# Kernel optimization log

Hardware: AMD Instinct MI355X
Metric: run time of the kernel (lower is better)

## Reference

```python
import jax, jax.numpy as jnp
import numpy as np

B, L, D = 128, 512, 512   # batch, len_max, encoder feature dim
E, H, V = 64, 512, 17     # label emb size, hidden size, label vocab
PAD = 0                   # entl_pad_value


def setup_inputs() -> dict:
    key = jax.random.key(0)
    ks = jax.random.split(key, 6)
    inputs = jax.random.normal(ks[0], (B, L, D), dtype=jnp.float32)
    emb_table = jax.random.normal(ks[1], (V, E), dtype=jnp.float32) * 0.02
    # xavier_uniform with tanh gain for ht1
    gain = 5.0 / 3.0
    limit1 = gain * np.sqrt(6.0 / (D + E + H))
    W1 = jax.random.uniform(ks[2], (H, D + E), dtype=jnp.float32,
                            minval=-limit1, maxval=limit1)
    b1 = jnp.zeros((H,), dtype=jnp.float32)
    limit2 = np.sqrt(1.0 / H)
    W2 = jax.random.uniform(ks[3], (V, H), dtype=jnp.float32,
                            minval=-limit2, maxval=limit2)
    b2 = jax.random.uniform(ks[4], (V,), dtype=jnp.float32,
                            minval=-limit2, maxval=limit2)
    return {"inputs": inputs, "emb_table": emb_table,
            "W1": W1, "b1": b1, "W2": W2, "b2": b2}


def reference(inputs, emb_table, W1, b1, W2, b2):
    # padding_idx row is identically zero (as in nn.Embedding(padding_idx=PAD))
    table = emb_table.at[PAD].set(0.0)

    def step(prev_emb, x_t):
        # x_t: [B, D], prev_emb: [B, E]
        x = jnp.concatenate([x_t, prev_emb], axis=-1)          # [B, D+E]
        h = jnp.tanh(x @ W1.T + b1)                            # [B, H]
        logit = h @ W2.T + b2                                  # [B, V]
        logp = jax.nn.log_softmax(logit, axis=-1)              # [B, V]
        pred = jnp.argmax(logp, axis=-1)                       # [B] int
        emb = table[pred]                                      # [B, E]
        return emb, (logit, pred, logp, emb)

    init_emb = jnp.broadcast_to(table[PAD], (inputs.shape[0], E))
    xs = jnp.swapaxes(inputs, 0, 1)                            # [L, B, D]
    _, (logits, preds, probs, preds_emb) = jax.lax.scan(step, init_emb, xs)
    # stack along time -> move time to dim 1
    logits = jnp.swapaxes(logits, 0, 1)       # [B, L, V]
    preds = jnp.swapaxes(preds, 0, 1)         # [B, L]
    probs = jnp.swapaxes(probs, 0, 1)         # [B, L, V]
    preds_emb = jnp.swapaxes(preds_emb, 0, 1) # [B, L, E]
    return logits, preds, probs, preds_emb
```

## Files before the change

kernel.cpp:

```cpp
#include <hip/hip_runtime.h>
#include <math.h>

#define B_ 128
#define L_ 512
#define D_ 512
#define E_ 64
#define H_ 512
#define V_ 17

#define LOG2E_F 1.4426950408889634f
#define LN2_F   0.6931471805599453f

__device__ __forceinline__ float fast_tanh(float x) {
  float e = __builtin_amdgcn_exp2f(x * (2.0f * LOG2E_F));
  return 1.0f - 2.0f * __builtin_amdgcn_rcpf(e + 1.0f);
}

__global__ void dh_kernel(const float* __restrict__ W1, const float* __restrict__ table,
                          float* __restrict__ TD) {
  int h = threadIdx.x;
  float w[E_];
#pragma unroll
  for (int e = 0; e < E_; ++e) w[e] = W1[h * (D_ + E_) + D_ + e];
  TD[h] = 0.f;
  for (int v = 1; v < V_; ++v) {
    float acc = 0.f;
#pragma unroll
    for (int e = 0; e < E_; ++e) acc += w[e] * table[v * E_ + e];
    TD[v * H_ + h] = fast_tanh(acc);
  }
}

#define PITCH 20
#define SCALE_A 1024.0f
#define SCALE_W 256.0f
#define INV_SCALE (1.0f / (1024.0f * 256.0f))

typedef _Float16 half8 __attribute__((ext_vector_type(8)));
typedef __fp16 fp16x2 __attribute__((ext_vector_type(2)));
typedef float float4v __attribute__((ext_vector_type(4)));

union H8c { half8 h; fp16x2 q[4]; unsigned int u[4]; uint4 u4; };

__device__ __forceinline__ uint4 split4(float4 v, float scale) {
  float a0 = v.x * scale, a1 = v.y * scale, a2 = v.z * scale, a3 = v.w * scale;
  _Float16 h0 = (_Float16)a0, h1 = (_Float16)a1, h2 = (_Float16)a2, h3 = (_Float16)a3;
  _Float16 l0 = (_Float16)(a0 - (float)h0), l1 = (_Float16)(a1 - (float)h1);
  _Float16 l2 = (_Float16)(a2 - (float)h2), l3 = (_Float16)(a3 - (float)h3);
  union { _Float16 h; unsigned short u; } c;
  unsigned int hu0, hu1, hu2, hu3, lu0, lu1, lu2, lu3;
  c.h = h0; hu0 = c.u; c.h = h1; hu1 = c.u; c.h = h2; hu2 = c.u; c.h = h3; hu3 = c.u;
  c.h = l0; lu0 = c.u; c.h = l1; lu1 = c.u; c.h = l2; lu2 = c.u; c.h = l3; lu3 = c.u;
  uint4 r;
  r.x = hu0 | (hu1 << 16);
  r.y = hu2 | (hu3 << 16);
  r.z = lu0 | (lu1 << 16);
  r.w = lu2 | (lu3 << 16);
  return r;
}

__device__ __forceinline__ uint2 pack4h(_Float16 a, _Float16 b, _Float16 c, _Float16 d) {
  union { _Float16 h; unsigned short u; } x;
  unsigned int lo, hi;
  x.h = a; lo = x.u; x.h = b; lo |= ((unsigned int)x.u) << 16;
  x.h = c; hi = x.u; x.h = d; hi |= ((unsigned int)x.u) << 16;
  return make_uint2(lo, hi);
}

__global__ __launch_bounds__(256)
void wsplit_kernel(const float* __restrict__ W1, unsigned int* __restrict__ WHI,
                   unsigned int* __restrict__ WLO) {
  const int idx = blockIdx.x * 256 + threadIdx.x;
  const int row = idx >> 7, c4 = idx & 127;
  const float4 wv = *(const float4*)&W1[(size_t)row * (D_ + E_) + 4 * c4];
  const uint4 pw = split4(wv, SCALE_W);
  *(uint2*)&WHI[row * 256 + 2 * c4] = make_uint2(pw.x, pw.y);
  *(uint2*)&WLO[row * 256 + 2 * c4] = make_uint2(pw.z, pw.w);
}

__global__ __launch_bounds__(512, 2)
void gemm_kernel(const float* __restrict__ A, const unsigned int* __restrict__ WHI,
                 const unsigned int* __restrict__ WLO,
                 const float* __restrict__ b1, float* __restrict__ TZ) {
  __shared__ unsigned int Ahi[128 * PITCH], Alo[128 * PITCH];
  __shared__ unsigned int Whi[512 * PITCH], Wlo[512 * PITCH];

  const int t = threadIdx.x;
  const int ln = t & 63, w = t >> 6;
  const int wm = w & 1, wn = w >> 1;
  const int mBase = blockIdx.x * 128;
  const int lrow = ln & 15, lquad = ln >> 4;

  float4v acc[4][8];
#pragma unroll
  for (int i = 0; i < 4; ++i)
#pragma unroll
    for (int j = 0; j < 8; ++j) acc[i][j] = (float4v){0.f, 0.f, 0.f, 0.f};

  for (int kt = 0; kt < D_; kt += 32) {
#pragma unroll
    for (int q = 0; q < 2; ++q) {
      const int idx = q * 512 + t;
      const int m = idx >> 3, f = idx & 7;
      const float4 av = *(const float4*)&A[(size_t)(mBase + m) * D_ + kt + 4 * f];
      const uint4 pa = split4(av, SCALE_A);
      *(uint2*)&Ahi[m * PITCH + 2 * f] = make_uint2(pa.x, pa.y);
      *(uint2*)&Alo[m * PITCH + 2 * f] = make_uint2(pa.z, pa.w);
    }
#pragma unroll
    for (int q = 0; q < 4; ++q) {
      const int idx = q * 512 + t;
      const int n = idx >> 2, d4 = (idx & 3) * 4;
      *(uint4*)&Whi[n * PITCH + d4] = *(const uint4*)&WHI[n * 256 + (kt >> 1) + d4];
      *(uint4*)&Wlo[n * PITCH + d4] = *(const uint4*)&WLO[n * 256 + (kt >> 1) + d4];
    }
    __syncthreads();

    half8 ah[4], al[4];
#pragma unroll
    for (int tm = 0; tm < 4; ++tm) {
      const int off = (wm * 64 + tm * 16 + lrow) * PITCH + 4 * lquad;
      ah[tm] = *(const half8*)&Ahi[off];
      al[tm] = *(const half8*)&Alo[off];
    }
#pragma unroll
    for (int tn = 0; tn < 8; ++tn) {
      const int off = (wn * 128 + tn * 16 + lrow) * PITCH + 4 * lquad;
      const half8 bh = *(const half8*)&Whi[off];
      const half8 bl = *(const half8*)&Wlo[off];
#pragma unroll
      for (int tm = 0; tm < 4; ++tm) {
        acc[tm][tn] = __builtin_amdgcn_mfma_f32_16x16x32_f16(ah[tm], bh, acc[tm][tn], 0, 0, 0);
        acc[tm][tn] = __builtin_amdgcn_mfma_f32_16x16x32_f16(ah[tm], bl, acc[tm][tn], 0, 0, 0);
        acc[tm][tn] = __builtin_amdgcn_mfma_f32_16x16x32_f16(al[tm], bh, acc[tm][tn], 0, 0, 0);
      }
    }
    __syncthreads();
  }

#pragma unroll
  for (int tn = 0; tn < 8; ++tn) {
    const int col = wn * 128 + tn * 16 + lrow;
    const float bv = b1[col];
#pragma unroll
    for (int tm = 0; tm < 4; ++tm) {
      const int row0 = mBase + wm * 64 + tm * 16 + lquad * 4;
#pragma unroll
      for (int r = 0; r < 4; ++r)
        TZ[(size_t)(row0 + r) * H_ + col] = fast_tanh(acc[tm][tn][r] * INV_SCALE + bv);
    }
  }
}

#define LGR 32
#define AP 520
#define WP 260

__global__ __launch_bounds__(512, 2)
void lg_kernel(const float* Zin, const float* __restrict__ TD,
               const float* __restrict__ W2, const float* __restrict__ b2,
               float* G) {
  __shared__ __align__(16) unsigned int sAhiD[LGR * AP / 2];
  __shared__ __align__(16) unsigned int sAloD[LGR * AP / 2];
  __shared__ __align__(16) unsigned int sUD[LGR * AP / 2];
  __shared__ __align__(16) unsigned int sTDd[V_ * 256];
  __shared__ __align__(16) unsigned int sW2hi[16 * WP];
  __shared__ __align__(16) unsigned int sW2lo[16 * WP];
  __shared__ __align__(16) unsigned int sW16hi[256];
  __shared__ __align__(16) unsigned int sW16lo[256];
  __shared__ __align__(16) float sS[8][16][20];
  __shared__ __align__(16) float sV16b[32];
  __shared__ __align__(16) unsigned char nb[LGR][20];

  const int t = threadIdx.x;
  const int ln = t & 63, w = t >> 6;
  const int bt0 = blockIdx.x * LGR;

#pragma unroll
  for (int i = 0; i < 8; ++i) {
    const int f = t + 512 * i;
    const int r = f >> 7, c4 = f & 127;
    const float4 z = *(const float4*)&Zin[(size_t)(bt0 + r) * H_ + 4 * c4];
    const float a0 = 1024.f * z.x, a1 = 1024.f * z.y, a2 = 1024.f * z.z, a3 = 1024.f * z.w;
    const _Float16 h0 = (_Float16)a0, h1 = (_Float16)a1, h2 = (_Float16)a2, h3 = (_Float16)a3;
    const _Float16 l0 = (_Float16)(a0 - (float)h0), l1 = (_Float16)(a1 - (float)h1);
    const _Float16 l2 = (_Float16)(a2 - (float)h2), l3 = (_Float16)(a3 - (float)h3);
    const _Float16 u0 = (_Float16)fmaf(-a0, z.x, 1024.f), u1 = (_Float16)fmaf(-a1, z.y, 1024.f);
    const _Float16 u2 = (_Float16)fmaf(-a2, z.z, 1024.f), u3 = (_Float16)fmaf(-a3, z.w, 1024.f);
    const int o = r * (AP / 2) + 2 * c4;
    *(uint2*)&sAhiD[o] = pack4h(h0, h1, h2, h3);
    *(uint2*)&sAloD[o] = pack4h(l0, l1, l2, l3);
    *(uint2*)&sUD[o]   = pack4h(u0, u1, u2, u3);
  }
#pragma unroll
  for (int i = 0; i < 5; ++i) {
    const int f = t + 512 * i;
    if (f < V_ * 128) {
      const int r = f >> 7, c4 = f & 127;
      const float4 d = *(const float4*)&TD[(size_t)r * H_ + 4 * c4];
      *(uint2*)&sTDd[r * 256 + 2 * c4] =
          pack4h((_Float16)d.x, (_Float16)d.y, (_Float16)d.z, (_Float16)d.w);
    }
  }
#pragma unroll
  for (int i = 0; i < 4; ++i) {
    const int f = t + 512 * i;
    const int r = f >> 7, c4 = f & 127;
    const float4 wv = *(const float4*)&W2[(size_t)r * H_ + 4 * c4];
    const uint4 pw = split4(wv, SCALE_W);
    *(uint2*)&sW2hi[r * WP + 2 * c4] = make_uint2(pw.x, pw.y);
    *(uint2*)&sW2lo[r * WP + 2 * c4] = make_uint2(pw.z, pw.w);
  }
  if (t < 128) {
    const float4 wv = *(const float4*)&W2[(size_t)16 * H_ + 4 * t];
    const uint4 pw = split4(wv, 1.0f);
    *(uint2*)&sW16hi[2 * t] = make_uint2(pw.x, pw.y);
    *(uint2*)&sW16lo[2 * t] = make_uint2(pw.z, pw.w);
  }
  __syncthreads();

  {
    const int row = t >> 4, seg = t & 15;
    const unsigned int* Ah = &sAhiD[row * (AP / 2) + seg * 16];
    const unsigned int* Al = &sAloD[row * (AP / 2) + seg * 16];
    const unsigned int* Wh = &sW16hi[seg * 16];
    const unsigned int* Wl = &sW16lo[seg * 16];
    float s = 0.f;
#pragma unroll
    for (int j = 0; j < 16; ++j) {
      const fp16x2 a = __builtin_bit_cast(fp16x2, Ah[j]);
      const fp16x2 l = __builtin_bit_cast(fp16x2, Al[j]);
      const fp16x2 wh = __builtin_bit_cast(fp16x2, Wh[j]);
      const fp16x2 wl = __builtin_bit_cast(fp16x2, Wl[j]);
      s = __builtin_amdgcn_fdot2(a, wh, s, false);
      s = __builtin_amdgcn_fdot2(l, wh, s, false);
      s = __builtin_amdgcn_fdot2(a, wl, s, false);
    }
    ((float*)sS)[row * 16 + seg] = s;
  }
  __syncthreads();
  if (t < 32) {
    float s = 0.f;
#pragma unroll
    for (int j = 0; j < 16; ++j) s += ((float*)sS)[t * 16 + j];
    sV16b[t] = s;
  }
  __syncthreads();

  const int lrow = ln & 15, lq = ln >> 4;
  const int rg = w & 1, pq = w >> 1;
  const int rbase = rg * 16;
  const float b2a = b2[lrow];
  const float b2c = b2[16];

  float4v acc[5];
  float p16s[5];
#pragma unroll
  for (int pi = 0; pi < 5; ++pi) { acc[pi] = (float4v){0.f, 0.f, 0.f, 0.f}; p16s[pi] = 0.f; }

  const _Float16* Ahalf = (const _Float16*)sAhiD;
  const _Float16* Alhalf = (const _Float16*)sAloD;
  const _Float16* Uhalf = (const _Float16*)sUD;
  const _Float16* TDhalf = (const _Float16*)sTDd;

  for (int kt = 0; kt < H_; kt += 32) {
    const int ho = kt + lq * 8;
    const half8 ahi = *(const half8*)(Ahalf + (rbase + lrow) * AP + ho);
    const half8 alo = *(const half8*)(Alhalf + (rbase + lrow) * AP + ho);
    const half8 uu  = *(const half8*)(Uhalf + (rbase + lrow) * AP + ho);
    const half8 tzv = ahi * (_Float16)0.0009765625f;
    H8c W16f; W16f.u4 = *(const uint4*)&sW16hi[ho >> 1];
    const int wo = lrow * WP + (kt >> 1) + lq * 4;
    const half8 bh0 = *(const half8*)&sW2hi[wo];
    const half8 bl0 = *(const half8*)&sW2lo[wo];
#pragma unroll
    for (int pi = 0; pi < 5; ++pi) {
      const int p = pq + 4 * pi;
      if (p < V_) {
        const half8 td = *(const half8*)(TDhalf + p * 512 + ho);
        const half8 q = tzv * td;
        const half8 s = q * q + ((_Float16)1.0f - q);
        const half8 dl = uu * (td * s);
        const half8 alp = alo + dl;
        acc[pi] = __builtin_amdgcn_mfma_f32_16x16x32_f16(ahi, bh0, acc[pi], 0, 0, 0);
        acc[pi] = __builtin_amdgcn_mfma_f32_16x16x32_f16(ahi, bl0, acc[pi], 0, 0, 0);
        acc[pi] = __builtin_amdgcn_mfma_f32_16x16x32_f16(alp, bh0, acc[pi], 0, 0, 0);
        H8c DL; DL.h = dl;
        p16s[pi] = __builtin_amdgcn_fdot2(DL.q[0], W16f.q[0], p16s[pi], false);
        p16s[pi] = __builtin_amdgcn_fdot2(DL.q[1], W16f.q[1], p16s[pi], false);
        p16s[pi] = __builtin_amdgcn_fdot2(DL.q[2], W16f.q[2], p16s[pi], false);
        p16s[pi] = __builtin_amdgcn_fdot2(DL.q[3], W16f.q[3], p16s[pi], false);
      }
    }
  }

#pragma unroll
  for (int pi = 0; pi < 5; ++pi) {
    const int p = pq + 4 * pi;
    if (p < V_) {
      float p16 = p16s[pi];
      p16 += __shfl_xor(p16, 16, 64);
      p16 += __shfl_xor(p16, 32, 64);
#pragma unroll
      for (int r = 0; r < 4; ++r)
        sS[w][lq * 4 + r][lrow] = acc[pi][r] * INV_SCALE + b2a;
      if (ln < 16) {
        float va[17];
        const float4 q0 = *(const float4*)&sS[w][ln][0];
        const float4 q1 = *(const float4*)&sS[w][ln][4];
        const float4 q2 = *(const float4*)&sS[w][ln][8];
        const float4 q3 = *(const float4*)&sS[w][ln][12];
        va[0] = q0.x; va[1] = q0.y; va[2] = q0.z; va[3] = q0.w;
        va[4] = q1.x; va[5] = q1.y; va[6] = q1.z; va[7] = q1.w;
        va[8] = q2.x; va[9] = q2.y; va[10] = q2.z; va[11] = q2.w;
        va[12] = q3.x; va[13] = q3.y; va[14] = q3.z; va[15] = q3.w;
        va[16] = (sV16b[rbase + ln] + p16) * 0.0009765625f + b2c;
        float m = va[0]; int am = 0;
#pragma unroll
        for (int i = 1; i < 17; ++i) if (va[i] > m) { m = va[i]; am = i; }
        float* gs = &G[(size_t)(bt0 + rbase + ln) * H_ + p * 20];
        *(float4*)&gs[0] = q0; *(float4*)&gs[4] = q1;
        *(float4*)&gs[8] = q2; *(float4*)&gs[12] = q3;
        gs[16] = va[16];
        nb[rbase + ln][p] = (unsigned char)am;
      }
    }
  }
  __syncthreads();
  if (t < 160) {
    const int row = t / 5, d = t % 5;
    ((unsigned int*)&G[(size_t)(bt0 + row) * H_ + 352])[d] =
        *(const unsigned int*)&nb[row][d * 4];
  }
}

__global__ __launch_bounds__(64, 1)
void chase_kernel(const float* __restrict__ G, float* __restrict__ out_preds) {
  __shared__ unsigned char nxt[L_ * 32];
  const int b = blockIdx.x, ln = threadIdx.x;
#pragma unroll
  for (int i = 0; i < 8; ++i) {
    const int tt = ln + 64 * i;
    const unsigned int* src = (const unsigned int*)&G[((size_t)b * L_ + tt) * H_ + 352];
    *(uint4*)&nxt[tt * 32] = *(const uint4*)src;
    *(unsigned int*)&nxt[tt * 32 + 16] = src[4];
  }
  __syncthreads();
  int pred = 0;
  float* op = out_preds + (size_t)b * L_;
  for (int tt = 0; tt < L_; ++tt) {
    pred = nxt[tt * 32 + pred];
    if (ln == 0) op[tt] = (float)pred;
  }
}

__global__ __launch_bounds__(256)
void epi_kernel(const float* __restrict__ G, const float* __restrict__ table,
                const float* __restrict__ preds,
                float* __restrict__ out_logits, float* __restrict__ out_probs,
                float* __restrict__ out_pemb) {
  const int bt = blockIdx.x * 256 + threadIdx.x;
  const int tt = bt & (L_ - 1);
  const int p = (tt == 0) ? 0 : (int)preds[bt - 1];
  const float* g = &G[(size_t)bt * H_ + p * 20];
  float va[17];
  {
    const float4 q0 = *(const float4*)&g[0];
    const float4 q1 = *(const float4*)&g[4];
    const float4 q2 = *(const float4*)&g[8];
    const float4 q3 = *(const float4*)&g[12];
    va[0] = q0.x; va[1] = q0.y; va[2] = q0.z; va[3] = q0.w;
    va[4] = q1.x; va[5] = q1.y; va[6] = q1.z; va[7] = q1.w;
    va[8] = q2.x; va[9] = q2.y; va[10] = q2.z; va[11] = q2.w;
    va[12] = q3.x; va[13] = q3.y; va[14] = q3.z; va[15] = q3.w;
    va[16] = g[16];
  }
  float m = va[0];
#pragma unroll
  for (int i = 1; i < 17; ++i) m = fmaxf(m, va[i]);
  float s = 0.f;
#pragma unroll
  for (int i = 0; i < 17; ++i) s += __builtin_amdgcn_exp2f((va[i] - m) * LOG2E_F);
  const float lse = __builtin_amdgcn_logf(s) * LN2_F;
  float* lo = out_logits + (size_t)bt * V_;
  float* pb = out_probs + (size_t)bt * V_;
#pragma unroll
  for (int i = 0; i < 17; ++i) { lo[i] = va[i]; pb[i] = va[i] - m - lse; }
  const int pr = (int)preds[bt];
  float* pe = out_pemb + (size_t)bt * E_;
  if (pr == 0) {
#pragma unroll
    for (int i = 0; i < 16; ++i) *(float4*)&pe[4 * i] = (float4){0.f, 0.f, 0.f, 0.f};
  } else {
    const float* tr = &table[(size_t)pr * E_];
#pragma unroll
    for (int i = 0; i < 16; ++i) *(float4*)&pe[4 * i] = *(const float4*)&tr[4 * i];
  }
}

extern "C" void kernel_launch(void* const* d_in, const int* in_sizes, int n_in,
                              void* d_out, int out_size, void* d_ws, size_t ws_size,
                              hipStream_t stream) {
  const float* inputs = (const float*)d_in[0];
  const float* table  = (const float*)d_in[1];
  const float* W1     = (const float*)d_in[2];
  const float* b1     = (const float*)d_in[3];
  const float* W2     = (const float*)d_in[4];
  const float* b2     = (const float*)d_in[5];

  float* out = (float*)d_out;
  float* out_logits = out;
  float* out_preds  = out_logits + (size_t)B_ * L_ * V_;
  float* out_probs  = out_preds + (size_t)B_ * L_;
  float* out_pemb   = out_probs + (size_t)B_ * L_ * V_;

  float* TD = (float*)d_ws;
  float* TZ = (float*)((char*)d_ws + 65536);

  unsigned int* WHI = (unsigned int*)out_pemb;
  unsigned int* WLO = WHI + 512 * 256;

  dh_kernel<<<1, 512, 0, stream>>>(W1, table, TD);
  wsplit_kernel<<<256, 256, 0, stream>>>(W1, WHI, WLO);
  gemm_kernel<<<512, 512, 0, stream>>>(inputs, WHI, WLO, b1, TZ);
  lg_kernel<<<65536 / LGR, 512, 0, stream>>>(TZ, TD, W2, b2, TZ);
  chase_kernel<<<B_, 64, 0, stream>>>(TZ, out_preds);
  epi_kernel<<<65536 / 256, 256, 0, stream>>>(TZ, table, out_preds,
                                              out_logits, out_probs, out_pemb);
}
```

Baseline: 502.4 us.

## Recast per-predecessor logit correction as a precomputed-weight MFMA GEMM

```diff
diff --git a/kernel.cpp b/kernel.cpp
--- a/kernel.cpp
+++ b/kernel.cpp
@@ -16,31 +16,14 @@
   return 1.0f - 2.0f * __builtin_amdgcn_rcpf(e + 1.0f);
 }
 
-__global__ void dh_kernel(const float* __restrict__ W1, const float* __restrict__ table,
-                          float* __restrict__ TD) {
-  int h = threadIdx.x;
-  float w[E_];
-#pragma unroll
-  for (int e = 0; e < E_; ++e) w[e] = W1[h * (D_ + E_) + D_ + e];
-  TD[h] = 0.f;
-  for (int v = 1; v < V_; ++v) {
-    float acc = 0.f;
-#pragma unroll
-    for (int e = 0; e < E_; ++e) acc += w[e] * table[v * E_ + e];
-    TD[v * H_ + h] = fast_tanh(acc);
-  }
-}
-
 #define PITCH 20
 #define SCALE_A 1024.0f
 #define SCALE_W 256.0f
 #define INV_SCALE (1.0f / (1024.0f * 256.0f))
+#define NC 304
 
 typedef _Float16 half8 __attribute__((ext_vector_type(8)));
-typedef __fp16 fp16x2 __attribute__((ext_vector_type(2)));
 typedef float float4v __attribute__((ext_vector_type(4)));
-
-union H8c { half8 h; fp16x2 q[4]; unsigned int u[4]; uint4 u4; };
 
 __device__ __forceinline__ uint4 split4(float4 v, float scale) {
   float a0 = v.x * scale, a1 = v.y * scale, a2 = v.z * scale, a3 = v.w * scale;
@@ -59,23 +42,61 @@
   return r;
 }
 
-__device__ __forceinline__ uint2 pack4h(_Float16 a, _Float16 b, _Float16 c, _Float16 d) {
-  union { _Float16 h; unsigned short u; } x;
-  unsigned int lo, hi;
-  x.h = a; lo = x.u; x.h = b; lo |= ((unsigned int)x.u) << 16;
-  x.h = c; hi = x.u; x.h = d; hi |= ((unsigned int)x.u) << 16;
-  return make_uint2(lo, hi);
+__device__ __forceinline__ unsigned int pack2h(float a, float b) {
+  union { _Float16 h; unsigned short u; } x, y;
+  x.h = (_Float16)a; y.h = (_Float16)b;
+  return (unsigned int)x.u | ((unsigned int)y.u << 16);
 }
 
 __global__ __launch_bounds__(256)
-void wsplit_kernel(const float* __restrict__ W1, unsigned int* __restrict__ WHI,
-                   unsigned int* __restrict__ WLO) {
-  const int idx = blockIdx.x * 256 + threadIdx.x;
-  const int row = idx >> 7, c4 = idx & 127;
-  const float4 wv = *(const float4*)&W1[(size_t)row * (D_ + E_) + 4 * c4];
-  const uint4 pw = split4(wv, SCALE_W);
-  *(uint2*)&WHI[row * 256 + 2 * c4] = make_uint2(pw.x, pw.y);
-  *(uint2*)&WLO[row * 256 + 2 * c4] = make_uint2(pw.z, pw.w);
+void prep_kernel(const float* __restrict__ W1, const float* __restrict__ W2,
+                 const float* __restrict__ table,
+                 unsigned int* __restrict__ WHI, unsigned int* __restrict__ WLO,
+                 unsigned int* __restrict__ W2HI, unsigned int* __restrict__ W2LO,
+                 unsigned int* __restrict__ Kp, unsigned int* __restrict__ K2p) {
+  const int bid = blockIdx.x, t = threadIdx.x;
+  if (bid < 256) {
+    const int idx = bid * 256 + t;
+    const int row = idx >> 7, c4 = idx & 127;
+    const float4 wv = *(const float4*)&W1[(size_t)row * (D_ + E_) + 4 * c4];
+    const uint4 pw = split4(wv, SCALE_W);
+    *(uint2*)&WHI[row * 256 + 2 * c4] = make_uint2(pw.x, pw.y);
+    *(uint2*)&WLO[row * 256 + 2 * c4] = make_uint2(pw.z, pw.w);
+  } else if (bid < 265) {
+    const int i = (bid - 256) * 256 + t;
+    if (i < V_ * 128) {
+      const int row = i >> 7, c4 = i & 127;
+      const float4 wv = *(const float4*)&W2[(size_t)row * H_ + 4 * c4];
+      const uint4 pw = split4(wv, SCALE_W);
+      *(uint2*)&W2HI[row * 256 + 2 * c4] = make_uint2(pw.x, pw.y);
+      *(uint2*)&W2LO[row * 256 + 2 * c4] = make_uint2(pw.z, pw.w);
+    }
+  } else {
+    const int c = bid - 265;
+    unsigned int o1 = 0, o2 = 0;
+    if (c < 289) {
+      const int p = c / 17, v = c - p * 17;
+      float k1[2], k2[2];
+#pragma unroll
+      for (int s = 0; s < 2; ++s) {
+        const int h = 2 * t + s;
+        float td = 0.f;
+        if (p > 0) {
+          float acc = 0.f;
+          for (int e = 0; e < E_; ++e)
+            acc += W1[(size_t)h * (D_ + E_) + D_ + e] * table[p * E_ + e];
+          td = fast_tanh(acc);
+        }
+        const float w2v = W2[(size_t)v * H_ + h];
+        k1[s] = 256.0f * td * w2v;
+        k2[s] = 65536.0f * td * td * w2v;
+      }
+      o1 = pack2h(k1[0], k1[1]);
+      o2 = pack2h(k2[0], k2[1]);
+    }
+    Kp[c * 256 + t] = o1;
+    K2p[c * 256 + t] = o2;
+  }
 }
 
 __global__ __launch_bounds__(512, 2)
@@ -152,185 +173,182 @@
   }
 }
 
-#define LGR 32
-#define AP 520
-#define WP 260
-
-__global__ __launch_bounds__(512, 2)
-void lg_kernel(const float* Zin, const float* __restrict__ TD,
-               const float* __restrict__ W2, const float* __restrict__ b2,
-               float* G) {
-  __shared__ __align__(16) unsigned int sAhiD[LGR * AP / 2];
-  __shared__ __align__(16) unsigned int sAloD[LGR * AP / 2];
-  __shared__ __align__(16) unsigned int sUD[LGR * AP / 2];
-  __shared__ __align__(16) unsigned int sTDd[V_ * 256];
-  __shared__ __align__(16) unsigned int sW2hi[16 * WP];
-  __shared__ __align__(16) unsigned int sW2lo[16 * WP];
-  __shared__ __align__(16) unsigned int sW16hi[256];
-  __shared__ __align__(16) unsigned int sW16lo[256];
-  __shared__ __align__(16) float sS[8][16][20];
-  __shared__ __align__(16) float sV16b[32];
-  __shared__ __align__(16) unsigned char nb[LGR][20];
+__global__ __launch_bounds__(512, 1)
+void glog_kernel(const float* Zin, const unsigned int* __restrict__ KpD,
+                 const unsigned int* __restrict__ K2D,
+                 const unsigned int* __restrict__ W2HI, const unsigned int* __restrict__ W2LO,
+                 const float* __restrict__ b2, float* G) {
+  __shared__ __align__(16) char pool[97408];
+  unsigned int* Ahi = (unsigned int*)pool;
+  unsigned int* Alo = Ahi + 2560;
+  unsigned int* Uf  = Alo + 2560;
+  unsigned int* A2f = Uf + 2560;
+  unsigned int* Bc  = A2f + 2560;
+  unsigned int* Bc2 = Bc + 6080;
+  unsigned int* Bh  = Bc2 + 6080;
+  unsigned int* Bl  = Bh + 640;
 
   const int t = threadIdx.x;
   const int ln = t & 63, w = t >> 6;
-  const int bt0 = blockIdx.x * LGR;
-
-#pragma unroll
-  for (int i = 0; i < 8; ++i) {
-    const int f = t + 512 * i;
-    const int r = f >> 7, c4 = f & 127;
-    const float4 z = *(const float4*)&Zin[(size_t)(bt0 + r) * H_ + 4 * c4];
-    const float a0 = 1024.f * z.x, a1 = 1024.f * z.y, a2 = 1024.f * z.z, a3 = 1024.f * z.w;
-    const _Float16 h0 = (_Float16)a0, h1 = (_Float16)a1, h2 = (_Float16)a2, h3 = (_Float16)a3;
-    const _Float16 l0 = (_Float16)(a0 - (float)h0), l1 = (_Float16)(a1 - (float)h1);
-    const _Float16 l2 = (_Float16)(a2 - (float)h2), l3 = (_Float16)(a3 - (float)h3);
-    const _Float16 u0 = (_Float16)fmaf(-a0, z.x, 1024.f), u1 = (_Float16)fmaf(-a1, z.y, 1024.f);
-    const _Float16 u2 = (_Float16)fmaf(-a2, z.z, 1024.f), u3 = (_Float16)fmaf(-a3, z.w, 1024.f);
-    const int o = r * (AP / 2) + 2 * c4;
-    *(uint2*)&sAhiD[o] = pack4h(h0, h1, h2, h3);
-    *(uint2*)&sAloD[o] = pack4h(l0, l1, l2, l3);
-    *(uint2*)&sUD[o]   = pack4h(u0, u1, u2, u3);
-  }
-#pragma unroll
-  for (int i = 0; i < 5; ++i) {
-    const int f = t + 512 * i;
-    if (f < V_ * 128) {
-      const int r = f >> 7, c4 = f & 127;
-      const float4 d = *(const float4*)&TD[(size_t)r * H_ + 4 * c4];
-      *(uint2*)&sTDd[r * 256 + 2 * c4] =
-          pack4h((_Float16)d.x, (_Float16)d.y, (_Float16)d.z, (_Float16)d.w);
-    }
-  }
-#pragma unroll
-  for (int i = 0; i < 4; ++i) {
-    const int f = t + 512 * i;
-    const int r = f >> 7, c4 = f & 127;
-    const float4 wv = *(const float4*)&W2[(size_t)r * H_ + 4 * c4];
-    const uint4 pw = split4(wv, SCALE_W);
-    *(uint2*)&sW2hi[r * WP + 2 * c4] = make_uint2(pw.x, pw.y);
-    *(uint2*)&sW2lo[r * WP + 2 * c4] = make_uint2(pw.z, pw.w);
-  }
-  if (t < 128) {
-    const float4 wv = *(const float4*)&W2[(size_t)16 * H_ + 4 * t];
-    const uint4 pw = split4(wv, 1.0f);
-    *(uint2*)&sW16hi[2 * t] = make_uint2(pw.x, pw.y);
-    *(uint2*)&sW16lo[2 * t] = make_uint2(pw.z, pw.w);
-  }
-  __syncthreads();
-
-  {
-    const int row = t >> 4, seg = t & 15;
-    const unsigned int* Ah = &sAhiD[row * (AP / 2) + seg * 16];
-    const unsigned int* Al = &sAloD[row * (AP / 2) + seg * 16];
-    const unsigned int* Wh = &sW16hi[seg * 16];
-    const unsigned int* Wl = &sW16lo[seg * 16];
-    float s = 0.f;
-#pragma unroll
-    for (int j = 0; j < 16; ++j) {
-      const fp16x2 a = __builtin_bit_cast(fp16x2, Ah[j]);
-      const fp16x2 l = __builtin_bit_cast(fp16x2, Al[j]);
-      const fp16x2 wh = __builtin_bit_cast(fp16x2, Wh[j]);
-      const fp16x2 wl = __builtin_bit_cast(fp16x2, Wl[j]);
-      s = __builtin_amdgcn_fdot2(a, wh, s, false);
-      s = __builtin_amdgcn_fdot2(l, wh, s, false);
-      s = __builtin_amdgcn_fdot2(a, wl, s, false);
-    }
-    ((float*)sS)[row * 16 + seg] = s;
-  }
-  __syncthreads();
-  if (t < 32) {
-    float s = 0.f;
-#pragma unroll
-    for (int j = 0; j < 16; ++j) s += ((float*)sS)[t * 16 + j];
-    sV16b[t] = s;
-  }
-  __syncthreads();
-
+  const int wm = w & 1, wn = w >> 1;
   const int lrow = ln & 15, lq = ln >> 4;
-  const int rg = w & 1, pq = w >> 1;
-  const int rbase = rg * 16;
-  const float b2a = b2[lrow];
-  const float b2c = b2[16];
-
-  float4v acc[5];
-  float p16s[5];
-#pragma unroll
-  for (int pi = 0; pi < 5; ++pi) { acc[pi] = (float4v){0.f, 0.f, 0.f, 0.f}; p16s[pi] = 0.f; }
-
-  const _Float16* Ahalf = (const _Float16*)sAhiD;
-  const _Float16* Alhalf = (const _Float16*)sAloD;
-  const _Float16* Uhalf = (const _Float16*)sUD;
-  const _Float16* TDhalf = (const _Float16*)sTDd;
+  const int bt0 = blockIdx.x * 128;
+
+  if (t < 300) { Bh[340 + t] = 0; Bl[340 + t] = 0; }
+
+  float4v accC[5][4];
+  float4v accB[2][4];
+#pragma unroll
+  for (int i = 0; i < 5; ++i)
+#pragma unroll
+    for (int mt = 0; mt < 4; ++mt) accC[i][mt] = (float4v){0.f, 0.f, 0.f, 0.f};
+#pragma unroll
+  for (int i = 0; i < 2; ++i)
+#pragma unroll
+    for (int mt = 0; mt < 4; ++mt) accB[i][mt] = (float4v){0.f, 0.f, 0.f, 0.f};
 
   for (int kt = 0; kt < H_; kt += 32) {
-    const int ho = kt + lq * 8;
-    const half8 ahi = *(const half8*)(Ahalf + (rbase + lrow) * AP + ho);
-    const half8 alo = *(const half8*)(Alhalf + (rbase + lrow) * AP + ho);
-    const half8 uu  = *(const half8*)(Uhalf + (rbase + lrow) * AP + ho);
-    const half8 tzv = ahi * (_Float16)0.0009765625f;
-    H8c W16f; W16f.u4 = *(const uint4*)&sW16hi[ho >> 1];
-    const int wo = lrow * WP + (kt >> 1) + lq * 4;
-    const half8 bh0 = *(const half8*)&sW2hi[wo];
-    const half8 bl0 = *(const half8*)&sW2lo[wo];
-#pragma unroll
-    for (int pi = 0; pi < 5; ++pi) {
-      const int p = pq + 4 * pi;
-      if (p < V_) {
-        const half8 td = *(const half8*)(TDhalf + p * 512 + ho);
-        const half8 q = tzv * td;
-        const half8 s = q * q + ((_Float16)1.0f - q);
-        const half8 dl = uu * (td * s);
-        const half8 alp = alo + dl;
-        acc[pi] = __builtin_amdgcn_mfma_f32_16x16x32_f16(ahi, bh0, acc[pi], 0, 0, 0);
-        acc[pi] = __builtin_amdgcn_mfma_f32_16x16x32_f16(ahi, bl0, acc[pi], 0, 0, 0);
-        acc[pi] = __builtin_amdgcn_mfma_f32_16x16x32_f16(alp, bh0, acc[pi], 0, 0, 0);
-        H8c DL; DL.h = dl;
-        p16s[pi] = __builtin_amdgcn_fdot2(DL.q[0], W16f.q[0], p16s[pi], false);
-        p16s[pi] = __builtin_amdgcn_fdot2(DL.q[1], W16f.q[1], p16s[pi], false);
-        p16s[pi] = __builtin_amdgcn_fdot2(DL.q[2], W16f.q[2], p16s[pi], false);
-        p16s[pi] = __builtin_amdgcn_fdot2(DL.q[3], W16f.q[3], p16s[pi], false);
-      }
-    }
-  }
-
-#pragma unroll
-  for (int pi = 0; pi < 5; ++pi) {
-    const int p = pq + 4 * pi;
-    if (p < V_) {
-      float p16 = p16s[pi];
-      p16 += __shfl_xor(p16, 16, 64);
-      p16 += __shfl_xor(p16, 32, 64);
-#pragma unroll
-      for (int r = 0; r < 4; ++r)
-        sS[w][lq * 4 + r][lrow] = acc[pi][r] * INV_SCALE + b2a;
-      if (ln < 16) {
-        float va[17];
-        const float4 q0 = *(const float4*)&sS[w][ln][0];
-        const float4 q1 = *(const float4*)&sS[w][ln][4];
-        const float4 q2 = *(const float4*)&sS[w][ln][8];
-        const float4 q3 = *(const float4*)&sS[w][ln][12];
-        va[0] = q0.x; va[1] = q0.y; va[2] = q0.z; va[3] = q0.w;
-        va[4] = q1.x; va[5] = q1.y; va[6] = q1.z; va[7] = q1.w;
-        va[8] = q2.x; va[9] = q2.y; va[10] = q2.z; va[11] = q2.w;
-        va[12] = q3.x; va[13] = q3.y; va[14] = q3.z; va[15] = q3.w;
-        va[16] = (sV16b[rbase + ln] + p16) * 0.0009765625f + b2c;
-        float m = va[0]; int am = 0;
-#pragma unroll
-        for (int i = 1; i < 17; ++i) if (va[i] > m) { m = va[i]; am = i; }
-        float* gs = &G[(size_t)(bt0 + rbase + ln) * H_ + p * 20];
-        *(float4*)&gs[0] = q0; *(float4*)&gs[4] = q1;
-        *(float4*)&gs[8] = q2; *(float4*)&gs[12] = q3;
-        gs[16] = va[16];
-        nb[rbase + ln][p] = (unsigned char)am;
-      }
-    }
-  }
-  __syncthreads();
-  if (t < 160) {
-    const int row = t / 5, d = t % 5;
-    ((unsigned int*)&G[(size_t)(bt0 + row) * H_ + 352])[d] =
-        *(const unsigned int*)&nb[row][d * 4];
+#pragma unroll
+    for (int i = 0; i < 2; ++i) {
+      const int idx = i * 512 + t;
+      const int m = idx >> 3, f = idx & 7;
+      const float4 z = *(const float4*)&Zin[(size_t)(bt0 + m) * H_ + kt + 4 * f];
+      const uint4 pa = split4(z, SCALE_A);
+      *(uint2*)&Ahi[m * PITCH + 2 * f] = make_uint2(pa.x, pa.y);
+      *(uint2*)&Alo[m * PITCH + 2 * f] = make_uint2(pa.z, pa.w);
+      const float u0 = fmaf(-z.x, z.x, 1.0f), u1 = fmaf(-z.y, z.y, 1.0f);
+      const float u2 = fmaf(-z.z, z.z, 1.0f), u3 = fmaf(-z.w, z.w, 1.0f);
+      *(uint2*)&Uf[m * PITCH + 2 * f] = make_uint2(pack2h(u0, u1), pack2h(u2, u3));
+      const float s2 = -1.0f / 256.0f;
+      *(uint2*)&A2f[m * PITCH + 2 * f] =
+          make_uint2(pack2h(u0 * z.x * s2, u1 * z.y * s2),
+                     pack2h(u2 * z.z * s2, u3 * z.w * s2));
+    }
+#pragma unroll
+    for (int i = 0; i < 3; ++i) {
+      const int idx = i * 512 + t;
+      if (idx < NC * 4) {
+        const int c = idx >> 2, g4 = (idx & 3) * 4;
+        *(uint4*)&Bc[c * PITCH + g4]  = *(const uint4*)&KpD[c * 256 + (kt >> 1) + g4];
+        *(uint4*)&Bc2[c * PITCH + g4] = *(const uint4*)&K2D[c * 256 + (kt >> 1) + g4];
+      }
+    }
+    if (t < 68) {
+      const int v = t >> 2, g4 = (t & 3) * 4;
+      *(uint4*)&Bh[v * PITCH + g4] = *(const uint4*)&W2HI[v * 256 + (kt >> 1) + g4];
+    } else if (t < 136) {
+      const int t2 = t - 68, v = t2 >> 2, g4 = (t2 & 3) * 4;
+      *(uint4*)&Bl[v * PITCH + g4] = *(const uint4*)&W2LO[v * 256 + (kt >> 1) + g4];
+    }
+    __syncthreads();
+
+    half8 fa_hi[4], fa_lo[4], fa_u[4], fa_a2[4];
+#pragma unroll
+    for (int mt = 0; mt < 4; ++mt) {
+      const int off = (wm * 64 + mt * 16 + lrow) * PITCH + 4 * lq;
+      fa_hi[mt] = *(const half8*)&Ahi[off];
+      fa_lo[mt] = *(const half8*)&Alo[off];
+      fa_u[mt]  = *(const half8*)&Uf[off];
+      fa_a2[mt] = *(const half8*)&A2f[off];
+    }
+#pragma unroll
+    for (int i = 0; i < 5; ++i) {
+      if (wn < 3 || i < 4) {
+        const int c = (wn * 5 + i) * 16 + lrow;
+        const half8 fb  = *(const half8*)&Bc[c * PITCH + 4 * lq];
+        const half8 fb2 = *(const half8*)&Bc2[c * PITCH + 4 * lq];
+#pragma unroll
+        for (int mt = 0; mt < 4; ++mt) {
+          accC[i][mt] = __builtin_amdgcn_mfma_f32_16x16x32_f16(fa_u[mt], fb, accC[i][mt], 0, 0, 0);
+          accC[i][mt] = __builtin_amdgcn_mfma_f32_16x16x32_f16(fa_a2[mt], fb2, accC[i][mt], 0, 0, 0);
+        }
+      }
+    }
+    if (wn == 3) {
+#pragma unroll
+      for (int bt2 = 0; bt2 < 2; ++bt2) {
+        const int off = (bt2 * 16 + lrow) * PITCH + 4 * lq;
+        const half8 bh = *(const half8*)&Bh[off];
+        const half8 bl = *(const half8*)&Bl[off];
+#pragma unroll
+        for (int mt = 0; mt < 4; ++mt) {
+          accB[bt2][mt] = __builtin_amdgcn_mfma_f32_16x16x32_f16(fa_hi[mt], bh, accB[bt2][mt], 0, 0, 0);
+          accB[bt2][mt] = __builtin_amdgcn_mfma_f32_16x16x32_f16(fa_hi[mt], bl, accB[bt2][mt], 0, 0, 0);
+          accB[bt2][mt] = __builtin_amdgcn_mfma_f32_16x16x32_f16(fa_lo[mt], bh, accB[bt2][mt], 0, 0, 0);
+        }
+      }
+    }
+    __syncthreads();
+  }
+
+  float* Gbuf = (float*)pool;
+  float* Bb   = Gbuf + 64 * 353;
+  float* sb2  = Bb + 64 * 21;
+  unsigned char* nbb = (unsigned char*)(sb2 + 20);
+
+  if (t < V_) sb2[t] = b2[t];
+
+#pragma unroll
+  for (int half = 0; half < 2; ++half) {
+    if (half) __syncthreads();
+    if (wm == half) {
+#pragma unroll
+      for (int i = 0; i < 5; ++i) {
+        if (wn < 3 || i < 4) {
+          const int c = (wn * 5 + i) * 16 + lrow;
+          if (c < 289) {
+            const int p = c / 17, v = c - p * 17;
+            const int j = p * 20 + v;
+#pragma unroll
+            for (int mt = 0; mt < 4; ++mt)
+#pragma unroll
+              for (int r = 0; r < 4; ++r)
+                Gbuf[(mt * 16 + lq * 4 + r) * 353 + j] = accC[i][mt][r] * (1.0f / 256.0f);
+          }
+        }
+      }
+      if (wn == 3) {
+#pragma unroll
+        for (int bt2 = 0; bt2 < 2; ++bt2) {
+          const int v = bt2 * 16 + lrow;
+          if (v < V_) {
+#pragma unroll
+            for (int mt = 0; mt < 4; ++mt)
+#pragma unroll
+              for (int r = 0; r < 4; ++r)
+                Bb[(mt * 16 + lq * 4 + r) * 21 + v] = accB[bt2][mt][r] * INV_SCALE;
+          }
+        }
+      }
+    }
+    __syncthreads();
+#pragma unroll
+    for (int k = 0; k < 3; ++k) {
+      const int task = k * 512 + t;
+      if (task < 1088) {
+        const int row = task & 63, p = task >> 6;
+        float g[17];
+#pragma unroll
+        for (int v = 0; v < V_; ++v)
+          g[v] = Gbuf[row * 353 + p * 20 + v] + Bb[row * 21 + v] + sb2[v];
+        float m = g[0]; int am = 0;
+#pragma unroll
+        for (int v = 1; v < V_; ++v) if (g[v] > m) { m = g[v]; am = v; }
+        float* gs = &G[(size_t)(bt0 + half * 64 + row) * H_ + p * 20];
+        *(float4*)&gs[0]  = make_float4(g[0], g[1], g[2], g[3]);
+        *(float4*)&gs[4]  = make_float4(g[4], g[5], g[6], g[7]);
+        *(float4*)&gs[8]  = make_float4(g[8], g[9], g[10], g[11]);
+        *(float4*)&gs[12] = make_float4(g[12], g[13], g[14], g[15]);
+        gs[16] = g[16];
+        nbb[row * 20 + p] = (unsigned char)am;
+      }
+    }
+    __syncthreads();
+    if (t < 320) {
+      const int row = t / 5, d = t % 5;
+      ((unsigned int*)&G[(size_t)(bt0 + half * 64 + row) * H_ + 352])[d] =
+          *(const unsigned int*)&nbb[row * 20 + 4 * d];
+    }
   }
 }
 
@@ -377,15 +395,15 @@
   }
   float m = va[0];
 #pragma unroll
-  for (int i = 1; i < 17; ++i) m = fmaxf(m, va[i]);
+  for (int i = 1; i < V_; ++i) m = fmaxf(m, va[i]);
   float s = 0.f;
 #pragma unroll
-  for (int i = 0; i < 17; ++i) s += __builtin_amdgcn_exp2f((va[i] - m) * LOG2E_F);
+  for (int i = 0; i < V_; ++i) s += __builtin_amdgcn_exp2f((va[i] - m) * LOG2E_F);
   const float lse = __builtin_amdgcn_logf(s) * LN2_F;
   float* lo = out_logits + (size_t)bt * V_;
   float* pb = out_probs + (size_t)bt * V_;
 #pragma unroll
-  for (int i = 0; i < 17; ++i) { lo[i] = va[i]; pb[i] = va[i] - m - lse; }
+  for (int i = 0; i < V_; ++i) { lo[i] = va[i]; pb[i] = va[i] - m - lse; }
   const int pr = (int)preds[bt];
   float* pe = out_pemb + (size_t)bt * E_;
   if (pr == 0) {
@@ -414,16 +432,18 @@
   float* out_probs  = out_preds + (size_t)B_ * L_;
   float* out_pemb   = out_probs + (size_t)B_ * L_ * V_;
 
-  float* TD = (float*)d_ws;
+  unsigned int* W2HI = (unsigned int*)d_ws;
+  unsigned int* W2LO = W2HI + V_ * 256;
   float* TZ = (float*)((char*)d_ws + 65536);
 
   unsigned int* WHI = (unsigned int*)out_pemb;
   unsigned int* WLO = WHI + 512 * 256;
-
-  dh_kernel<<<1, 512, 0, stream>>>(W1, table, TD);
-  wsplit_kernel<<<256, 256, 0, stream>>>(W1, WHI, WLO);
+  unsigned int* Kp  = (unsigned int*)out_probs;
+  unsigned int* K2p = Kp + NC * 256;
+
+  prep_kernel<<<569, 256, 0, stream>>>(W1, W2, table, WHI, WLO, W2HI, W2LO, Kp, K2p);
   gemm_kernel<<<512, 512, 0, stream>>>(inputs, WHI, WLO, b1, TZ);
-  lg_kernel<<<65536 / LGR, 512, 0, stream>>>(TZ, TD, W2, b2, TZ);
+  glog_kernel<<<512, 512, 0, stream>>>(TZ, Kp, K2p, W2HI, W2LO, b2, TZ);
   chase_kernel<<<B_, 64, 0, stream>>>(TZ, out_preds);
   epi_kernel<<<65536 / 256, 256, 0, stream>>>(TZ, table, out_preds,
                                               out_logits, out_probs, out_pemb);
```

After: 463.2 us. -7.8%, faster.
